# Performance work log

Hardware: AMD Instinct MI355X
Metric: run time of the kernel (lower is better)

The kernel has to match this reference:

```python
import jax, jax.numpy as jnp
import numpy as np

D = 2048
N = 4096
HEAD = 2
DH = D // HEAD


def setup_inputs() -> dict:
    key = jax.random.key(0)
    ks = jax.random.split(key, 7)
    s = 0.02  # realistic init scale for weights
    x = jax.random.normal(ks[0], (1, N, D), jnp.float32)
    Wq1 = jax.random.normal(ks[1], (DH, DH), jnp.float32) * s
    Wq2 = jax.random.normal(ks[2], (DH, DH), jnp.float32) * s
    Wk1 = jax.random.normal(ks[3], (DH, DH), jnp.float32) * s
    Wk2 = jax.random.normal(ks[4], (DH, DH), jnp.float32) * s
    Wv1 = jax.random.normal(ks[5], (DH, DH), jnp.float32) * s
    Wv2 = jax.random.normal(ks[6], (DH, DH), jnp.float32) * s
    return {"x": x, "Wq1": Wq1, "Wq2": Wq2, "Wk1": Wk1, "Wk2": Wk2,
            "Wv1": Wv1, "Wv2": Wv2}


def _head(xh, Wq, Wk, Wv):
    # xh: [1, N, Dh]; Linear applies in @ W^T (no bias)
    q = (xh @ Wq.T)[0]                      # [N, Dh]
    k = (xh @ Wk.T)[0]                      # [N, Dh] (k reshaped to 2D in torch)
    v = (xh @ Wv.T)[0]                      # [N, Dh]
    # QK_T linear with weight dynamically set to k (detached in torch):
    Sc = q @ jax.lax.stop_gradient(k).T     # [N, N]
    # Sc_V linear on v^T with weight set to Sc (detached in torch):
    Sc = jax.lax.stop_gradient(Sc)
    return v.T @ Sc.T                       # [Dh, N]  == (Sc @ v)^T


def reference(x, Wq1, Wq2, Wk1, Wk2, Wv1, Wv2):
    Dh = Wq1.shape[0]
    x1, x2 = x[..., :Dh], x[..., Dh:]       # torch.chunk(x, 2, dim=2)
    o1 = _head(x1, Wq1, Wk1, Wv1)           # [Dh, N]
    o2 = _head(x2, Wq2, Wk2, Wv2)           # [Dh, N]
    out = jnp.concatenate([o1, o2], axis=0).T  # transpose(-2,-1).squeeze -> [N, D]
    return out
```

## Files before the change

kernel.cpp:

```cpp
#include <hip/hip_runtime.h>
#include <hip/hip_bf16.h>


using bf16 = __hip_bfloat16;
typedef __attribute__((ext_vector_type(8))) __bf16 bf16x8;
typedef __attribute__((ext_vector_type(8))) unsigned short u16x8;
typedef __attribute__((ext_vector_type(4))) float f32x4;

#define M1 (1024 * 1024)

struct GB {
    const bf16* A[20];
    const bf16* B[20];
    void*       C[20];
    int lda[20];
    int ldb[20];
};

__device__ __forceinline__ void gload_lds16(const void* g, void* l) {
    __builtin_amdgcn_global_load_lds(
        (const __attribute__((address_space(1))) void*)g,
        (__attribute__((address_space(3))) void*)l, 16, 0, 0);
}

__device__ __forceinline__ void storeC(bf16* C, size_t idx, float v) {
    C[idx] = __float2bfloat16(v);
}
__device__ __forceinline__ void storeC(float* C, size_t idx, float v) {
    C[idx] = v;
}

template<int BM_, int BN_, typename OUT_T>
__global__ __launch_bounds__(256, 4)
void gemm_bt_pa(GB g, int Ksub, int ldc)
{
    const int gx = gridDim.x, gy = gridDim.y;
    const int nwg = gx * gy * gridDim.z;
    const int orig = blockIdx.x + gx * (blockIdx.y + gy * blockIdx.z);
    const int cpx = nwg >> 3;
    const int wg = (orig & 7) * cpx + (orig >> 3);
    const int bx = wg % gx;
    const int by = (wg / gx) % gy;
    const int bz = wg / (gx * gy);

    const bf16* __restrict__ A = g.A[bz];
    const bf16* __restrict__ B = g.B[bz];
    OUT_T* __restrict__ C = (OUT_T*)g.C[bz];
    const int lda = g.lda[bz];
    const int ldb = g.ldb[bz];

    __shared__ unsigned short As[BM_ * 32];
    __shared__ unsigned short Bs[BN_ * 32];

    constexpr int MI = BM_ / 32;
    constexpr int NI = BN_ / 32;

    const int tid  = threadIdx.x;
    const int lane = tid & 63;
    const int wave = tid >> 6;
    const int wm   = wave >> 1;
    const int wn   = wave & 1;

    const int m0 = by * BM_;
    const int n0 = bx * BN_;

    const int fr = lane & 15;
    const int kg = lane >> 4;

    const int srow = tid >> 2;
    const int scol = (tid & 3) * 8;

    f32x4 acc[MI][NI];
    #pragma unroll
    for (int i = 0; i < MI; ++i)
        #pragma unroll
        for (int j = 0; j < NI; ++j)
            acc[i][j] = {0.f, 0.f, 0.f, 0.f};

    for (int kt = 0; kt < Ksub; kt += 32) {
        #pragma unroll
        for (int r = 0; r < BM_ / 64; ++r) {
            const bf16* gA = A + (size_t)(m0 + r * 64 + srow) * lda + (kt + scol);
            gload_lds16(gA, &As[(r * 64 + srow) * 32 + scol]);
        }
        #pragma unroll
        for (int r = 0; r < BN_ / 64; ++r) {
            const bf16* gB = B + (size_t)(n0 + r * 64 + srow) * ldb + (kt + scol);
            gload_lds16(gB, &Bs[(r * 64 + srow) * 32 + scol]);
        }
        __syncthreads();

        bf16x8 afrag[MI], bfrag[NI];
        #pragma unroll
        for (int mi = 0; mi < MI; ++mi)
            afrag[mi] = *(const bf16x8*)&As[(wm * (BM_ / 2) + mi * 16 + fr) * 32 + kg * 8];
        #pragma unroll
        for (int ni = 0; ni < NI; ++ni)
            bfrag[ni] = *(const bf16x8*)&Bs[(wn * (BN_ / 2) + ni * 16 + fr) * 32 + kg * 8];

        #pragma unroll
        for (int mi = 0; mi < MI; ++mi)
            #pragma unroll
            for (int ni = 0; ni < NI; ++ni)
                acc[mi][ni] = __builtin_amdgcn_mfma_f32_16x16x32_bf16(
                    afrag[mi], bfrag[ni], acc[mi][ni], 0, 0, 0);
        __syncthreads();
    }

    #pragma unroll
    for (int mi = 0; mi < MI; ++mi) {
        #pragma unroll
        for (int ni = 0; ni < NI; ++ni) {
            const int col = n0 + wn * (BN_ / 2) + ni * 16 + fr;
            #pragma unroll
            for (int j = 0; j < 4; ++j) {
                const int row = m0 + wm * (BM_ / 2) + mi * 16 + kg * 4 + j;
                storeC(C, (size_t)row * ldc + col, acc[mi][ni][j]);
            }
        }
    }
}


__device__ __forceinline__ ushort4 cvt4(float4 v) {
    ushort4 o; bf16 h;
    h = __float2bfloat16(v.x); o.x = *(unsigned short*)&h;
    h = __float2bfloat16(v.y); o.y = *(unsigned short*)&h;
    h = __float2bfloat16(v.z); o.z = *(unsigned short*)&h;
    h = __float2bfloat16(v.w); o.w = *(unsigned short*)&h;
    return o;
}

struct PrepArgs {
    const float* x;
    const float* w[4];
    const float* wv[2];
    bf16* xb;
    bf16* xt;
    bf16* wdst;
};

__device__ void xpose64(const float* __restrict__ src, int ldsrc,
                        int r0, int c0,
                        bf16* __restrict__ dstS, int ldS,
                        bf16* __restrict__ dstT, int ldT,
                        float (*tile)[65], int t)
{
    const int tr  = t >> 4;
    const int tc4 = (t & 15) * 4;
    #pragma unroll
    for (int ph = 0; ph < 4; ++ph) {
        const int row = ph * 16 + tr;
        float4 v = *(const float4*)(src + (size_t)(r0 + row) * ldsrc + c0 + tc4);
        tile[row][tc4 + 0] = v.x;
        tile[row][tc4 + 1] = v.y;
        tile[row][tc4 + 2] = v.z;
        tile[row][tc4 + 3] = v.w;
        if (dstS)
            *(ushort4*)((unsigned short*)dstS + (size_t)(r0 + row) * ldS + c0 + tc4) = cvt4(v);
    }
    __syncthreads();
    #pragma unroll
    for (int ph = 0; ph < 4; ++ph) {
        const int crow = ph * 16 + tr;
        float4 v = {tile[tc4 + 0][crow], tile[tc4 + 1][crow],
                    tile[tc4 + 2][crow], tile[tc4 + 3][crow]};
        *(ushort4*)((unsigned short*)dstT + (size_t)(c0 + crow) * ldT + r0 + tc4) = cvt4(v);
    }
}

__global__ void prep(PrepArgs p)
{
    __shared__ float tile[64][65];
    const int b = blockIdx.x;
    const int t = threadIdx.x;

    if (b < 2048) {
        const int n0 = (b & 63) * 64;
        const int c0 = (b >> 6) * 64;
        xpose64(p.x, 2048, n0, c0, p.xb, 2048, p.xt, 4096, tile, t);
    } else if (b < 3072) {
        const int i = b - 2048;
        const int mat = i >> 8;
        const int tl  = i & 255;
        const int r0 = (tl & 15) * 64;
        const int c0 = (tl >> 4) * 64;
        xpose64(p.w[mat], 1024, r0, c0, nullptr, 0,
                p.wdst + (size_t)mat * M1, 1024, tile, t);
    } else {
        const int i = b - 3072;
        const int mat = i >> 9;
        const int blk = i & 511;
        const size_t off = (size_t)blk * 2048 + t * 8;
        float4 v0 = *(const float4*)(p.wv[mat] + off);
        float4 v1 = *(const float4*)(p.wv[mat] + off + 4);
        unsigned short* d = (unsigned short*)p.wdst + (size_t)(4 + mat) * M1 + off;
        *(ushort4*)d       = cvt4(v0);
        *(ushort4*)(d + 4) = cvt4(v1);
    }
}


__device__ __forceinline__ void reduce_slices(const unsigned short* src,
                                              unsigned short* dst,
                                              int h, int r, int nslice)
{
    float acc[8] = {0, 0, 0, 0, 0, 0, 0, 0};
    for (int s = 0; s < nslice; ++s) {
        u16x8 v = *(const u16x8*)(src + ((size_t)(h * nslice + s) << 20) + r);
        #pragma unroll
        for (int j = 0; j < 8; ++j)
            acc[j] += __uint_as_float(((unsigned)v[j]) << 16);
    }
    u16x8 o;
    #pragma unroll
    for (int j = 0; j < 8; ++j) {
        bf16 hh = __float2bfloat16(acc[j]);
        o[j] = *(unsigned short*)&hh;
    }
    *(u16x8*)(dst + ((size_t)h << 20) + r) = o;
}

__global__ void reduce_GM(const unsigned short* Gp, const unsigned short* Mp,
                          unsigned short* Gd, unsigned short* Md)
{
    const int b = blockIdx.x, t = threadIdx.x;
    if (b < 1024) {
        const int e = (b * 256 + t) * 8;
        reduce_slices(Gp, Gd, e >> 20, e & (M1 - 1), 8);
    } else {
        const int e = ((b - 1024) * 256 + t) * 8;
        reduce_slices(Mp, Md, e >> 20, e & (M1 - 1), 2);
    }
}

__global__ void reduce_4(const unsigned short* Sp, unsigned short* Dd)
{
    const int e = (blockIdx.x * 256 + threadIdx.x) * 8;
    reduce_slices(Sp, Dd, e >> 20, e & (M1 - 1), 4);
}


extern "C" void kernel_launch(void* const* d_in, const int* in_sizes, int n_in,
                              void* d_out, int out_size, void* d_ws, size_t ws_size,
                              hipStream_t stream)
{
    bf16* xb   = (bf16*)d_ws;
    bf16* xt   = xb + 8 * M1;
    bf16* wdst = xt + 8 * M1;
    bf16* Mp   = wdst + 6 * M1;
    bf16* Mb   = Mp + 4 * M1;
    bf16* Gb   = Mb + 2 * M1;
    bf16* Ytb  = Gb + 2 * M1;
    bf16* Utb  = Ytb + 2 * M1;

    bf16* scr = (bf16*)d_out;

    PrepArgs pa;
    pa.x = (const float*)d_in[0];
    pa.w[0] = (const float*)d_in[1];  pa.w[1] = (const float*)d_in[2];
    pa.w[2] = (const float*)d_in[3];  pa.w[3] = (const float*)d_in[4];
    pa.wv[0] = (const float*)d_in[5]; pa.wv[1] = (const float*)d_in[6];
    pa.xb = xb; pa.xt = xt; pa.wdst = wdst;
    prep<<<4096, 256, 0, stream>>>(pa);

    GB g;

    for (int z = 0; z < 16; ++z) {
        const int h = z >> 3, s = z & 7;
        g.A[z] = xt + (size_t)h * 4 * M1 + s * 512;  g.lda[z] = 4096;
        g.B[z] = g.A[z];                             g.ldb[z] = 4096;
        g.C[z] = (bf16*)scr + (size_t)z * M1;
    }
    for (int z = 16; z < 20; ++z) {
        const int j = z - 16, h = j >> 1, s = j & 1;
        g.A[z] = wdst + (size_t)h * M1 + s * 512;           g.lda[z] = 1024;
        g.B[z] = wdst + (size_t)(2 + h) * M1 + s * 512;     g.ldb[z] = 1024;
        g.C[z] = Mp + (size_t)j * M1;
    }
    gemm_bt_pa<128, 128, bf16><<<dim3(8, 8, 20), 256, 0, stream>>>(g, 512, 1024);

    reduce_GM<<<2048, 256, 0, stream>>>((const unsigned short*)scr, (const unsigned short*)Mp,
                                        (unsigned short*)Gb, (unsigned short*)Mb);

    for (int z = 0; z < 8; ++z) {
        const int h = z >> 2, s = z & 3;
        g.A[z] = Mb + (size_t)h * M1 + s * 256;  g.lda[z] = 1024;
        g.B[z] = Gb + (size_t)h * M1 + s * 256;  g.ldb[z] = 1024;
        g.C[z] = (bf16*)scr + (size_t)z * M1;
    }
    gemm_bt_pa<128, 128, bf16><<<dim3(8, 8, 8), 256, 0, stream>>>(g, 256, 1024);

    reduce_4<<<1024, 256, 0, stream>>>((const unsigned short*)scr, (unsigned short*)Ytb);

    for (int z = 0; z < 8; ++z) {
        const int h = z >> 2, s = z & 3;
        g.A[z] = wdst + (size_t)(4 + h) * M1 + s * 256;  g.lda[z] = 1024;
        g.B[z] = Ytb + (size_t)h * M1 + s * 256;         g.ldb[z] = 1024;
        g.C[z] = (bf16*)scr + (size_t)z * M1;
    }
    gemm_bt_pa<128, 128, bf16><<<dim3(8, 8, 8), 256, 0, stream>>>(g, 256, 1024);

    reduce_4<<<1024, 256, 0, stream>>>((const unsigned short*)scr, (unsigned short*)Utb);

    for (int z = 0; z < 2; ++z) {
        g.A[z] = xb + (size_t)z * 1024;   g.lda[z] = 2048;
        g.B[z] = Utb + (size_t)z * M1;    g.ldb[z] = 1024;
        g.C[z] = (float*)d_out + (size_t)z * 1024;
    }
    gemm_bt_pa<128, 64, float><<<dim3(16, 32, 2), 256, 0, stream>>>(g, 1024, 2048);
}
```

Measured before the change: 126.7 us.

## Reassociate attention chain and fuse independent GEMMs into heterogeneous grouped launches

Reorders the matrix-product chain: x·Mᵀ is computed as a separate product Qp, and the Wv·G product runs in the same launch, so one GEMM plus reduce_4 pair disappears. A heterogeneous grouped GEMM kernel with per-problem ldc, K split and block offsets replaces the uniform 3D grid. This cuts one launch and one split-K reduction pass. In exchange it writes a larger intermediate Qp (8M elements) and adds a linear search per block to find its problem.

Result: slower. 139.2 us (+9.8%).

```diff
diff --git a/kernel.cpp b/kernel.cpp
--- a/kernel.cpp
+++ b/kernel.cpp
@@ -9,12 +9,15 @@
 
 #define M1 (1024 * 1024)
 
-struct GB {
+struct GBH {
     const bf16* A[20];
     const bf16* B[20];
     void*       C[20];
-    int lda[20];
-    int ldb[20];
+    int lda[20], ldb[20], ldc[20];
+    int gxl[20];
+    int ksub[20];
+    int blk_off[21];
+    int nz;
 };
 
 __device__ __forceinline__ void gload_lds16(const void* g, void* l) {
@@ -32,22 +35,26 @@
 
 template<int BM_, int BN_, typename OUT_T>
 __global__ __launch_bounds__(256, 4)
-void gemm_bt_pa(GB g, int Ksub, int ldc)
-{
-    const int gx = gridDim.x, gy = gridDim.y;
-    const int nwg = gx * gy * gridDim.z;
-    const int orig = blockIdx.x + gx * (blockIdx.y + gy * blockIdx.z);
+void gemm_bt_h(GBH g, int nwg)
+{
+    const int orig = blockIdx.x;
     const int cpx = nwg >> 3;
     const int wg = (orig & 7) * cpx + (orig >> 3);
-    const int bx = wg % gx;
-    const int by = (wg / gx) % gy;
-    const int bz = wg / (gx * gy);
-
-    const bf16* __restrict__ A = g.A[bz];
-    const bf16* __restrict__ B = g.B[bz];
-    OUT_T* __restrict__ C = (OUT_T*)g.C[bz];
-    const int lda = g.lda[bz];
-    const int ldb = g.ldb[bz];
+
+    int z = 0;
+    while (z + 1 < g.nz && wg >= g.blk_off[z + 1]) ++z;
+    const int local = wg - g.blk_off[z];
+    const int gxl = g.gxl[z];
+    const int bx = local & ((1 << gxl) - 1);
+    const int by = local >> gxl;
+
+    const bf16* __restrict__ A = g.A[z];
+    const bf16* __restrict__ B = g.B[z];
+    OUT_T* __restrict__ C = (OUT_T*)g.C[z];
+    const int lda = g.lda[z];
+    const int ldb = g.ldb[z];
+    const int ldc = g.ldc[z];
+    const int Ksub = g.ksub[z];
 
     __shared__ unsigned short As[BM_ * 32];
     __shared__ unsigned short Bs[BN_ * 32];
@@ -249,10 +256,10 @@
     bf16* xt   = xb + 8 * M1;
     bf16* wdst = xt + 8 * M1;
     bf16* Mp   = wdst + 6 * M1;
-    bf16* Mb   = Mp + 4 * M1;
-    bf16* Gb   = Mb + 2 * M1;
-    bf16* Ytb  = Gb + 2 * M1;
-    bf16* Utb  = Ytb + 2 * M1;
+    bf16* Mtb  = Mp + 4 * M1;
+    bf16* Gb   = Mtb + 2 * M1;
+    bf16* Qp   = Gb + 2 * M1;
+    bf16* Ztb  = Qp + 8 * M1;
 
     bf16* scr = (bf16*)d_out;
 
@@ -264,49 +271,52 @@
     pa.xb = xb; pa.xt = xt; pa.wdst = wdst;
     prep<<<4096, 256, 0, stream>>>(pa);
 
-    GB g;
+    GBH g;
 
     for (int z = 0; z < 16; ++z) {
         const int h = z >> 3, s = z & 7;
         g.A[z] = xt + (size_t)h * 4 * M1 + s * 512;  g.lda[z] = 4096;
         g.B[z] = g.A[z];                             g.ldb[z] = 4096;
-        g.C[z] = (bf16*)scr + (size_t)z * M1;
+        g.C[z] = (bf16*)scr + (size_t)z * M1;        g.ldc[z] = 1024;
+        g.gxl[z] = 3; g.ksub[z] = 512; g.blk_off[z] = z * 64;
     }
     for (int z = 16; z < 20; ++z) {
         const int j = z - 16, h = j >> 1, s = j & 1;
-        g.A[z] = wdst + (size_t)h * M1 + s * 512;           g.lda[z] = 1024;
-        g.B[z] = wdst + (size_t)(2 + h) * M1 + s * 512;     g.ldb[z] = 1024;
-        g.C[z] = Mp + (size_t)j * M1;
-    }
-    gemm_bt_pa<128, 128, bf16><<<dim3(8, 8, 20), 256, 0, stream>>>(g, 512, 1024);
+        g.A[z] = wdst + (size_t)(2 + h) * M1 + s * 512;  g.lda[z] = 1024;
+        g.B[z] = wdst + (size_t)h * M1 + s * 512;        g.ldb[z] = 1024;
+        g.C[z] = Mp + (size_t)j * M1;                    g.ldc[z] = 1024;
+        g.gxl[z] = 3; g.ksub[z] = 512; g.blk_off[z] = z * 64;
+    }
+    g.blk_off[20] = 1280; g.nz = 20;
+    gemm_bt_h<128, 128, bf16><<<1280, 256, 0, stream>>>(g, 1280);
 
     reduce_GM<<<2048, 256, 0, stream>>>((const unsigned short*)scr, (const unsigned short*)Mp,
-                                        (unsigned short*)Gb, (unsigned short*)Mb);
-
-    for (int z = 0; z < 8; ++z) {
-        const int h = z >> 2, s = z & 3;
-        g.A[z] = Mb + (size_t)h * M1 + s * 256;  g.lda[z] = 1024;
-        g.B[z] = Gb + (size_t)h * M1 + s * 256;  g.ldb[z] = 1024;
-        g.C[z] = (bf16*)scr + (size_t)z * M1;
-    }
-    gemm_bt_pa<128, 128, bf16><<<dim3(8, 8, 8), 256, 0, stream>>>(g, 256, 1024);
-
-    reduce_4<<<1024, 256, 0, stream>>>((const unsigned short*)scr, (unsigned short*)Ytb);
-
-    for (int z = 0; z < 8; ++z) {
-        const int h = z >> 2, s = z & 3;
+                                        (unsigned short*)Gb, (unsigned short*)Mtb);
+
+    for (int h = 0; h < 2; ++h) {
+        g.A[h] = xb + (size_t)h * 1024;        g.lda[h] = 2048;
+        g.B[h] = Mtb + (size_t)h * M1;         g.ldb[h] = 1024;
+        g.C[h] = Qp + (size_t)h * 4 * M1;      g.ldc[h] = 1024;
+        g.gxl[h] = 3; g.ksub[h] = 1024; g.blk_off[h] = h * 256;
+    }
+    for (int z = 2; z < 10; ++z) {
+        const int j = z - 2, h = j >> 2, s = j & 3;
         g.A[z] = wdst + (size_t)(4 + h) * M1 + s * 256;  g.lda[z] = 1024;
-        g.B[z] = Ytb + (size_t)h * M1 + s * 256;         g.ldb[z] = 1024;
-        g.C[z] = (bf16*)scr + (size_t)z * M1;
-    }
-    gemm_bt_pa<128, 128, bf16><<<dim3(8, 8, 8), 256, 0, stream>>>(g, 256, 1024);
-
-    reduce_4<<<1024, 256, 0, stream>>>((const unsigned short*)scr, (unsigned short*)Utb);
-
-    for (int z = 0; z < 2; ++z) {
-        g.A[z] = xb + (size_t)z * 1024;   g.lda[z] = 2048;
-        g.B[z] = Utb + (size_t)z * M1;    g.ldb[z] = 1024;
-        g.C[z] = (float*)d_out + (size_t)z * 1024;
-    }
-    gemm_bt_pa<128, 64, float><<<dim3(16, 32, 2), 256, 0, stream>>>(g, 1024, 2048);
-}
+        g.B[z] = Gb + (size_t)h * M1 + s * 256;          g.ldb[z] = 1024;
+        g.C[z] = (bf16*)scr + (size_t)j * M1;            g.ldc[z] = 1024;
+        g.gxl[z] = 3; g.ksub[z] = 256; g.blk_off[z] = 512 + j * 64;
+    }
+    g.blk_off[10] = 1024; g.nz = 10;
+    gemm_bt_h<128, 128, bf16><<<1024, 256, 0, stream>>>(g, 1024);
+
+    reduce_4<<<1024, 256, 0, stream>>>((const unsigned short*)scr, (unsigned short*)Ztb);
+
+    for (int h = 0; h < 2; ++h) {
+        g.A[h] = Qp + (size_t)h * 4 * M1;      g.lda[h] = 1024;
+        g.B[h] = Ztb + (size_t)h * M1;         g.ldb[h] = 1024;
+        g.C[h] = (float*)d_out + (size_t)h * 1024;  g.ldc[h] = 2048;
+        g.gxl[h] = 4; g.ksub[h] = 1024; g.blk_off[h] = h * 512;
+    }
+    g.blk_off[2] = 1024; g.nz = 2;
+    gemm_bt_h<128, 64, float><<<1024, 256, 0, stream>>>(g, 1024);
+}
```

## Double-buffer LDS tiles with async prefetch of next K-slice in GEMM

Applied to the files above, without the earlier changes.

Converts the GEMM main loop to double-buffered shared memory. The next K tile is issued via global_load_lds before the current one is consumed, and a partial vmcnt wait lets only the older loads complete. The aim is to hide global-memory latency behind the MFMA work. It doubles LDS use, which may reduce occupancy, and it relies on hand-written waitcnt counts, which only cover NLOADS values of 3 or 4 and otherwise fall back to a full wait.

Result: no change. 128.3 us (+1.2%).

```diff
diff --git a/kernel.cpp b/kernel.cpp
--- a/kernel.cpp
+++ b/kernel.cpp
@@ -21,6 +21,13 @@
     __builtin_amdgcn_global_load_lds(
         (const __attribute__((address_space(1))) void*)g,
         (__attribute__((address_space(3))) void*)l, 16, 0, 0);
+}
+
+template<int N>
+__device__ __forceinline__ void waitv() {
+    if constexpr (N == 4)      asm volatile("s_waitcnt vmcnt(4)" ::: "memory");
+    else if constexpr (N == 3) asm volatile("s_waitcnt vmcnt(3)" ::: "memory");
+    else                       asm volatile("s_waitcnt vmcnt(0)" ::: "memory");
 }
 
 __device__ __forceinline__ void storeC(bf16* C, size_t idx, float v) {
@@ -49,11 +56,12 @@
     const int lda = g.lda[bz];
     const int ldb = g.ldb[bz];
 
-    __shared__ unsigned short As[BM_ * 32];
-    __shared__ unsigned short Bs[BN_ * 32];
+    __shared__ unsigned short As[2][BM_ * 32];
+    __shared__ unsigned short Bs[2][BN_ * 32];
 
     constexpr int MI = BM_ / 32;
     constexpr int NI = BN_ / 32;
+    constexpr int NLOADS = (BM_ + BN_) / 64;
 
     const int tid  = threadIdx.x;
     const int lane = tid & 63;
@@ -70,6 +78,17 @@
     const int srow = tid >> 2;
     const int scol = (tid & 3) * 8;
 
+    auto stage = [&](int buf, int kt) {
+        #pragma unroll
+        for (int r = 0; r < BM_ / 64; ++r)
+            gload_lds16(A + (size_t)(m0 + r * 64 + srow) * lda + (kt + scol),
+                        &As[buf][(r * 64 + srow) * 32 + scol]);
+        #pragma unroll
+        for (int r = 0; r < BN_ / 64; ++r)
+            gload_lds16(B + (size_t)(n0 + r * 64 + srow) * ldb + (kt + scol),
+                        &Bs[buf][(r * 64 + srow) * 32 + scol]);
+    };
+
     f32x4 acc[MI][NI];
     #pragma unroll
     for (int i = 0; i < MI; ++i)
@@ -77,26 +96,27 @@
         for (int j = 0; j < NI; ++j)
             acc[i][j] = {0.f, 0.f, 0.f, 0.f};
 
-    for (int kt = 0; kt < Ksub; kt += 32) {
-        #pragma unroll
-        for (int r = 0; r < BM_ / 64; ++r) {
-            const bf16* gA = A + (size_t)(m0 + r * 64 + srow) * lda + (kt + scol);
-            gload_lds16(gA, &As[(r * 64 + srow) * 32 + scol]);
+    const int niter = Ksub >> 5;
+    int cur = 0;
+    stage(0, 0);
+
+    for (int it = 0; it < niter; ++it) {
+        if (it + 1 < niter) {
+            stage(cur ^ 1, (it + 1) << 5);
+            waitv<NLOADS>();
+        } else {
+            waitv<0>();
         }
-        #pragma unroll
-        for (int r = 0; r < BN_ / 64; ++r) {
-            const bf16* gB = B + (size_t)(n0 + r * 64 + srow) * ldb + (kt + scol);
-            gload_lds16(gB, &Bs[(r * 64 + srow) * 32 + scol]);
-        }
-        __syncthreads();
+        __builtin_amdgcn_s_barrier();
+        __builtin_amdgcn_sched_barrier(0);
 
         bf16x8 afrag[MI], bfrag[NI];
         #pragma unroll
         for (int mi = 0; mi < MI; ++mi)
-            afrag[mi] = *(const bf16x8*)&As[(wm * (BM_ / 2) + mi * 16 + fr) * 32 + kg * 8];
+            afrag[mi] = *(const bf16x8*)&As[cur][(wm * (BM_ / 2) + mi * 16 + fr) * 32 + kg * 8];
         #pragma unroll
         for (int ni = 0; ni < NI; ++ni)
-            bfrag[ni] = *(const bf16x8*)&Bs[(wn * (BN_ / 2) + ni * 16 + fr) * 32 + kg * 8];
+            bfrag[ni] = *(const bf16x8*)&Bs[cur][(wn * (BN_ / 2) + ni * 16 + fr) * 32 + kg * 8];
 
         #pragma unroll
         for (int mi = 0; mi < MI; ++mi)
@@ -104,7 +124,11 @@
             for (int ni = 0; ni < NI; ++ni)
                 acc[mi][ni] = __builtin_amdgcn_mfma_f32_16x16x32_bf16(
                     afrag[mi], bfrag[ni], acc[mi][ni], 0, 0, 0);
-        __syncthreads();
+
+        __builtin_amdgcn_sched_barrier(0);
+        __builtin_amdgcn_s_barrier();
+        __builtin_amdgcn_sched_barrier(0);
+        cur ^= 1;
     }
 
     #pragma unroll
```
